# Optimization experiments

Hardware: AMD Instinct MI355X
Metric: run time of the kernel (lower is better)

## Reference

```python
import jax, jax.numpy as jnp
import numpy as np

N = 10000      # nodes
E = 160000     # edges
C = 72         # hidden dim = 18 * mul (mul=4)
A = 16         # node_attr dim (16x0e)
L = 3          # layers
O = 64         # output dim (64x0e)
B = 16         # graphs in batch
IN_DIM = 18    # irreps_node_input dim
SH = 9         # spherical harmonics dim, lmax=2
FC = 100       # radial MLP hidden (fc_neurons=[1,100])
MAX_RADIUS = 2.0
NUM_NEIGHBORS = 16.0
NUM_NODES = 625.0


def sph_harm_l2(d):
    # component-normalized real spherical harmonics up to l=2 on unit vectors d [E,3]
    x, y, z = d[:, 0], d[:, 1], d[:, 2]
    s3, s5, s15 = 3.0 ** 0.5, 5.0 ** 0.5, 15.0 ** 0.5
    return jnp.stack([
        jnp.ones_like(x),
        s3 * x, s3 * y, s3 * z,
        s15 * x * y, s15 * y * z, (s5 / 2.0) * (3.0 * z * z - 1.0),
        s15 * x * z, (s15 / 2.0) * (x * x - y * y),
    ], axis=1)  # [E, 9]


def setup_inputs() -> dict:
    key = jax.random.key(0)
    ks = jax.random.split(key, 16)
    pos = jax.random.normal(ks[0], (N, 3), dtype=jnp.float32)
    node_attr = jax.random.normal(ks[1], (N, A), dtype=jnp.float32)
    batch = jnp.sort(jax.random.randint(ks[2], (N,), 0, B))
    edge_src = jax.random.randint(ks[3], (E,), 0, N)
    edge_dst = jax.random.randint(ks[4], (E,), 0, N)
    W_in = jax.random.normal(ks[5], (IN_DIM, C), dtype=jnp.float32) / np.sqrt(IN_DIM)
    W_tp = jax.random.normal(ks[6], (L, SH, C, C), dtype=jnp.float32) / np.sqrt(C)
    W_self = jax.random.normal(ks[7], (L, C, C), dtype=jnp.float32) / np.sqrt(C)
    W_attr = jax.random.normal(ks[8], (L, A, C), dtype=jnp.float32) / np.sqrt(A)
    fc1_w = jax.random.normal(ks[9], (L, 1, FC), dtype=jnp.float32)
    fc1_b = jnp.zeros((L, FC), dtype=jnp.float32)
    fc2_w = jax.random.normal(ks[10], (L, FC, SH), dtype=jnp.float32) / np.sqrt(FC)
    W_out = jax.random.normal(ks[11], (C, O), dtype=jnp.float32) / np.sqrt(C)
    return {"pos": pos, "node_attr": node_attr, "batch": batch,
            "edge_src": edge_src, "edge_dst": edge_dst,
            "W_in": W_in, "W_tp": W_tp, "W_self": W_self, "W_attr": W_attr,
            "fc1_w": fc1_w, "fc1_b": fc1_b, "fc2_w": fc2_w, "W_out": W_out}


def reference(pos, node_attr, batch, edge_src, edge_dst,
              W_in, W_tp, W_self, W_attr, fc1_w, fc1_b, fc2_w, W_out):
    n = pos.shape[0]
    # edge geometry
    rvec = pos[edge_src] - pos[edge_dst]                      # [E,3]
    r = jnp.linalg.norm(rvec, axis=1, keepdims=True)          # [E,1]
    dvec = rvec / jnp.maximum(r, 1e-9)
    sh = sph_harm_l2(dvec)                                    # [E,9]
    # single cosine radial basis with cutoff at max_radius (number_of_basis=1)
    t = r / MAX_RADIUS
    emb = jnp.where(t < 1.0, jnp.cos(0.5 * jnp.pi * t), 0.0)  # [E,1]
    # node inputs: fixed one-hot on the scalar channel, embedded to hidden dim
    onehot = jnp.zeros((IN_DIM,), dtype=pos.dtype).at[0].set(1.0)
    h = jnp.broadcast_to((onehot @ W_in)[None, :], (n, C))    # [N,C]
    for l in range(L):
        # radial MLP -> per-edge, per-SH-path weights
        u = jax.nn.silu(emb @ fc1_w[l] + fc1_b[l]) @ fc2_w[l]  # [E,9]
        path = u * sh                                          # [E,9]
        hs = h[edge_src]                                       # [E,C]
        m = jnp.zeros_like(hs)
        for s in range(SH):  # fixed small set of tensor-product paths
            m = m + path[:, s:s + 1] * (hs @ W_tp[l, s])       # [E,C]
        agg = jax.ops.segment_sum(m, edge_dst, num_segments=n) / np.sqrt(NUM_NEIGHBORS)
        h = jax.nn.gelu(agg + h @ W_self[l] + node_attr @ W_attr[l])
    out_nodes = h @ W_out                                      # [N,O]
    pooled = jax.ops.segment_sum(out_nodes, batch, num_segments=B)
    return pooled / np.sqrt(NUM_NODES)                         # [B,O]
```

## Files before the change

kernel.cpp:

```cpp
#include <hip/hip_runtime.h>
#include <math.h>

#define NN 10000
#define NE 160000
#define CC 72
#define AA 16
#define LL 3
#define OO 64
#define NBATCH 16
#define SH 9
#define FCN 100
#define KK (SH*CC)
#define KA 736
#define KP 768
#define KG 96
#define NT 5
#define PSTRIDE 12
#define NB 1024
#define EMAX 176

typedef __attribute__((ext_vector_type(8))) short bf16x8;
typedef __attribute__((ext_vector_type(4))) float f32x4;

static __device__ __forceinline__ float gelu_tanh(float x) {
    float x3 = x * x * x;
    float inner = 0.7978845608028654f * (x + 0.044715f * x3);
    return 0.5f * x * (1.0f + tanhf(inner));
}
static __device__ __forceinline__ unsigned short f2bf(float x) {
    unsigned int u = __float_as_uint(x);
    u += 0x7FFFu + ((u >> 16) & 1u);
    return (unsigned short)(u >> 16);
}
static __device__ __forceinline__ float bf2f(unsigned short u) {
    return __uint_as_float((unsigned int)u << 16);
}

#define GB_HIST 625
#define GB_UTAB 13
#define GB_WCAT 180
#define GB_INIT 704
#define GB_PREP (GB_HIST + GB_UTAB + GB_WCAT + GB_INIT)

__global__ __launch_bounds__(256) void k_prep(
        const float* __restrict__ pos, const int* __restrict__ esrc,
        const int* __restrict__ edst, int* __restrict__ cnt,
        const float* __restrict__ fc1w, const float* __restrict__ fc1b,
        const float* __restrict__ fc2w, float* __restrict__ U,
        const float* __restrict__ Wtp, const float* __restrict__ Wself,
        const float* __restrict__ Wattr, unsigned short* __restrict__ Wb,
        const float* __restrict__ W_in, unsigned short* __restrict__ h0) {
    int bb = blockIdx.x, t = threadIdx.x;
    if (bb < GB_HIST) {
        int e = bb * 256 + t;
        if (e < NE) {
            int s = esrc[e], d = edst[e];
            float dx = pos[3 * s] - pos[3 * d];
            float dy = pos[3 * s + 1] - pos[3 * d + 1];
            float dz = pos[3 * s + 2] - pos[3 * d + 2];
            float r = sqrtf(dx * dx + dy * dy + dz * dz);
            if (r * 0.5f < 1.0f) atomicAdd(&cnt[d], 1);
        }
        return;
    }
    bb -= GB_HIST;
    if (bb < GB_UTAB) {
        int i = bb * 256 + t;
        if (i < LL * (NB + 1)) {
            int l = i / (NB + 1), b = i - l * (NB + 1);
            float emb = cosf(1.5707963267948966f * ((float)b / (float)NB));
            float u[SH];
#pragma unroll
            for (int q = 0; q < SH; ++q) u[q] = 0.f;
            const float* w1 = &fc1w[l * FCN];
            const float* b1 = &fc1b[l * FCN];
            const float* w2 = &fc2w[l * FCN * SH];
            for (int f = 0; f < FCN; ++f) {
                float a = emb * w1[f] + b1[f];
                float si = a / (1.0f + expf(-a));
#pragma unroll
                for (int q = 0; q < SH; ++q) u[q] += si * w2[f * SH + q];
            }
            float* ud = &U[(size_t)i * 12];
#pragma unroll
            for (int q = 0; q < SH; ++q) ud[q] = u[q];
            ud[9] = 0.f; ud[10] = 0.f; ud[11] = 0.f;
        }
        return;
    }
    bb -= GB_UTAB;
    if (bb < GB_WCAT) {
        int i0 = (bb * 256 + t) * 4;
#pragma unroll
        for (int u = 0; u < 4; ++u) {
            int i = i0 + u;
            int l = i / (NT * KG * 128);
            int rem = i - l * (NT * KG * 128);
            int nt = rem / (KG * 128); rem -= nt * (KG * 128);
            int kg = rem / 128; int e = rem - kg * 128;
            int n = nt * 16 + (e >> 3);
            int k = kg * 8 + (e & 7);
            float v = 0.f;
            if (n < CC && k < KA) {
                if (k < KK)            v = 0.25f * Wtp[(size_t)l * KK * CC + k * CC + n];
                else if (k < KK + CC)  v = Wself[(size_t)l * CC * CC + (k - KK) * CC + n];
                else                   v = Wattr[(size_t)l * AA * CC + (k - KK - CC) * CC + n];
            }
            Wb[i] = f2bf(v);
        }
        return;
    }
    bb -= GB_WCAT;
    {
        int i0 = (bb * 256 + t) * 4;
#pragma unroll
        for (int u = 0; u < 4; ++u) {
            int i = i0 + u;
            if (i < NN * CC) h0[i] = f2bf(W_in[i % CC]);
        }
    }
}

__global__ void k_scan(const int* __restrict__ cnt, int* __restrict__ off) {
    __shared__ int sa[256], sb[256];
    const int PER = 40;
    int t = threadIdx.x;
    int base = t * PER;
    int loc[PER];
    int run = 0;
#pragma unroll
    for (int i = 0; i < PER; ++i) {
        int idx = base + i;
        int v = (idx < NN) ? cnt[idx] : 0;
        loc[i] = run;
        run += v;
    }
    sa[t] = run;
    __syncthreads();
    int* in = sa; int* out = sb;
    for (int o = 1; o < 256; o <<= 1) {
        int v = in[t];
        if (t >= o) v += in[t - o];
        out[t] = v;
        __syncthreads();
        int* tmp = in; in = out; out = tmp;
    }
    int ebase = (t > 0) ? in[t - 1] : 0;
#pragma unroll
    for (int i = 0; i < PER; ++i) {
        int idx = base + i;
        if (idx <= NN) off[idx] = ebase + loc[i];
    }
}

__global__ void k_scatter2(const float* __restrict__ pos, const int* __restrict__ esrc,
                           const int* __restrict__ edst, const int* __restrict__ off,
                           int* __restrict__ cur, int* __restrict__ src_s,
                           int* __restrict__ dst_s) {
    int e = blockIdx.x * blockDim.x + threadIdx.x;
    if (e >= NE) return;
    int s = esrc[e], d = edst[e];
    float dx = pos[3 * s] - pos[3 * d];
    float dy = pos[3 * s + 1] - pos[3 * d + 1];
    float dz = pos[3 * s + 2] - pos[3 * d + 2];
    float r = sqrtf(dx * dx + dy * dy + dz * dz);
    if (r * 0.5f < 1.0f) {
        int slot = off[d] + atomicAdd(&cur[d], 1);
        src_s[slot] = s;
        dst_s[slot] = d;
    }
}

__global__ __launch_bounds__(256) void k_path2(const float* __restrict__ pos,
                                               const int* __restrict__ src_s,
                                               const int* __restrict__ dst_s,
                                               const float* __restrict__ U,
                                               const int* __restrict__ off,
                                               float* __restrict__ path) {
    int slot = blockIdx.x * blockDim.x + threadIdx.x;
    if (slot >= off[NN]) return;
    int s = src_s[slot], d = dst_s[slot];
    float dx = pos[3 * s] - pos[3 * d];
    float dy = pos[3 * s + 1] - pos[3 * d + 1];
    float dz = pos[3 * s + 2] - pos[3 * d + 2];
    float r = sqrtf(dx * dx + dy * dy + dz * dz);
    float inv = 1.0f / fmaxf(r, 1e-9f);
    float x = dx * inv, y = dy * inv, z = dz * inv;
    const float s3 = 1.7320508075688772f;
    const float s5 = 2.23606797749979f;
    const float s15 = 3.872983346207417f;
    float sh[SH];
    sh[0] = 1.0f;
    sh[1] = s3 * x;
    sh[2] = s3 * y;
    sh[3] = s3 * z;
    sh[4] = s15 * x * y;
    sh[5] = s15 * y * z;
    sh[6] = 0.5f * s5 * (3.0f * z * z - 1.0f);
    sh[7] = s15 * x * z;
    sh[8] = 0.5f * s15 * (x * x - y * y);

    float fb = r * 0.5f * (float)NB;
    int b0 = (int)fb;
    float fr = fb - (float)b0;

#pragma unroll
    for (int l = 0; l < LL; ++l) {
        const float* t0 = &U[((size_t)l * (NB + 1) + b0) * 12];
        float4 a0 = *(const float4*)(t0 + 0);
        float4 a1 = *(const float4*)(t0 + 4);
        float  a2 = t0[8];
        float4 c0 = *(const float4*)(t0 + 12);
        float4 c1 = *(const float4*)(t0 + 16);
        float  c2 = t0[20];
        float u0 = a0.x + fr * (c0.x - a0.x);
        float u1 = a0.y + fr * (c0.y - a0.y);
        float u2 = a0.z + fr * (c0.z - a0.z);
        float u3 = a0.w + fr * (c0.w - a0.w);
        float u4 = a1.x + fr * (c1.x - a1.x);
        float u5 = a1.y + fr * (c1.y - a1.y);
        float u6 = a1.z + fr * (c1.z - a1.z);
        float u7 = a1.w + fr * (c1.w - a1.w);
        float u8 = a2   + fr * (c2   - a2);
        float* pd = &path[((size_t)l * NE + slot) * PSTRIDE];
        *(float4*)(pd + 0) = make_float4(u0 * sh[0], u1 * sh[1], u2 * sh[2], u3 * sh[3]);
        *(float4*)(pd + 4) = make_float4(u4 * sh[4], u5 * sh[5], u6 * sh[6], u7 * sh[7]);
        *(float4*)(pd + 8) = make_float4(u8 * sh[8], 0.f, 0.f, 0.f);
    }
}

__global__ __launch_bounds__(1024, 8) void k_layer(
        const unsigned short* __restrict__ h,
        const float* __restrict__ attr,
        const float* __restrict__ path_l,
        const int* __restrict__ src_s,
        const int* __restrict__ off,
        const unsigned short* __restrict__ Wb,
        unsigned short* __restrict__ hout) {
    __shared__ float Plds[EMAX * PSTRIDE];
    __shared__ unsigned short Alds[KG * 128];
    int t = threadIdx.x, w = t >> 6, lane = t & 63;
    int n0 = blockIdx.x * 16;
    int d = n0 + w;
    int b0 = off[n0], e0 = off[n0 + 16];
    int db = off[d], de = off[d + 1];

    float a1[SH], a2[SH];
#pragma unroll
    for (int q = 0; q < SH; ++q) { a1[q] = 0.f; a2[q] = 0.f; }
    bool two = lane < (CC - 64);

    for (int base = b0; base < e0; base += EMAX) {
        int nE = min(EMAX, e0 - base);
        const float4* p4 = (const float4*)(path_l + (size_t)base * PSTRIDE);
        for (int idx = t; idx < nE * 3; idx += 1024)
            *(float4*)&Plds[idx * 4] = p4[idx];
        __syncthreads();
        int lb = db > base ? db : base;
        int le = de < base + nE ? de : base + nE;
        for (int i = lb; i < le; i += 4) {
            int m = le - i;
            float h1v[4], h2v[4];
#pragma unroll
            for (int j = 0; j < 4; ++j) {
                if (j < m) {
                    int s = src_s[i + j];
                    h1v[j] = bf2f(h[(size_t)s * CC + lane]);
                    h2v[j] = two ? bf2f(h[(size_t)s * CC + 64 + lane]) : 0.f;
                }
            }
#pragma unroll
            for (int j = 0; j < 4; ++j) {
                if (j < m) {
                    const float* p = &Plds[(i + j - base) * PSTRIDE];
                    float4 p0 = *(const float4*)p;
                    float4 p1 = *(const float4*)(p + 4);
                    float p8 = p[8];
                    float hv1 = h1v[j], hv2 = h2v[j];
                    a1[0] += p0.x * hv1; a2[0] += p0.x * hv2;
                    a1[1] += p0.y * hv1; a2[1] += p0.y * hv2;
                    a1[2] += p0.z * hv1; a2[2] += p0.z * hv2;
                    a1[3] += p0.w * hv1; a2[3] += p0.w * hv2;
                    a1[4] += p1.x * hv1; a2[4] += p1.x * hv2;
                    a1[5] += p1.y * hv1; a2[5] += p1.y * hv2;
                    a1[6] += p1.z * hv1; a2[6] += p1.z * hv2;
                    a1[7] += p1.w * hv1; a2[7] += p1.w * hv2;
                    a1[8] += p8 * hv1;   a2[8] += p8 * hv2;
                }
            }
        }
        __syncthreads();
    }

    unsigned short* At = Alds + w * 8;
    int kgc = lane >> 3, kjc = lane & 7;
#pragma unroll
    for (int q = 0; q < SH; ++q) {
        At[(9 * q + kgc) * 128 + kjc] = f2bf(a1[q]);
        if (two) At[(9 * q + 8) * 128 + lane] = f2bf(a2[q]);
    }
    At[(81 + kgc) * 128 + kjc] = h[(size_t)d * CC + lane];
    if (two) At[89 * 128 + lane] = h[(size_t)d * CC + 64 + lane];
    if (lane < AA) At[(90 + (lane >> 3)) * 128 + (lane & 7)] = f2bf(attr[(size_t)d * AA + lane]);
    if (lane < 32) At[(92 + (lane >> 3)) * 128 + (lane & 7)] = 0;
    __syncthreads();

    if (w < NT) {
        const unsigned short* Ab = Alds + (lane & 15) * 8;
        const unsigned short* Bb = Wb + ((size_t)w * KG) * 128 + (lane & 15) * 8;
        f32x4 acc = (f32x4){0.f, 0.f, 0.f, 0.f};
#pragma unroll
        for (int s = 0; s < 24; ++s) {
            int kg = s * 4 + (lane >> 4);
            bf16x8 af = *(const bf16x8*)(Ab + (size_t)kg * 128);
            bf16x8 bq = *(const bf16x8*)(Bb + (size_t)kg * 128);
            acc = __builtin_amdgcn_mfma_f32_16x16x32_bf16(af, bq, acc, 0, 0, 0);
        }
        int cb = lane & 15, rb = (lane >> 4) * 4;
        int row = n0 + rb, col = w * 16 + cb;
        if (col < CC) {
#pragma unroll
            for (int j = 0; j < 4; ++j)
                hout[(size_t)(row + j) * CC + col] = f2bf(gelu_tanh(acc[j]));
        }
    }
}

__global__ __launch_bounds__(256) void k_pool(const unsigned short* __restrict__ h,
                                              const int* __restrict__ batch,
                                              float* __restrict__ hp) {
    __shared__ float sp[NBATCH * CC];
    int t = threadIdx.x;
    for (int i = t; i < NBATCH * CC; i += 256) sp[i] = 0.f;
    __syncthreads();
    int n0 = blockIdx.x * 16;
    for (int i = t; i < 16 * CC; i += 256) {
        int nl = i / CC, c = i - nl * CC;
        int n = n0 + nl;
        if (n < NN) atomicAdd(&sp[batch[n] * CC + c], bf2f(h[(size_t)n * CC + c]));
    }
    __syncthreads();
    for (int i = t; i < NBATCH * CC; i += 256) {
        float v = sp[i];
        if (v != 0.f) atomicAdd(&hp[i], v);
    }
}

__global__ __launch_bounds__(1024) void k_outmm(const float* __restrict__ hp,
                                                const float* __restrict__ Wout,
                                                float* __restrict__ out) {
    __shared__ float hs[NBATCH * CC];
    int t = threadIdx.x;
    for (int i = t; i < NBATCH * CC; i += 1024) hs[i] = hp[i];
    __syncthreads();
    int b = t >> 6, o = t & 63;
    float acc = 0.f;
#pragma unroll 8
    for (int c = 0; c < CC; ++c) acc += hs[b * CC + c] * Wout[c * OO + o];
    out[t] = acc * (1.0f / 25.0f);
}

extern "C" void kernel_launch(void* const* d_in, const int* in_sizes, int n_in,
                              void* d_out, int out_size, void* d_ws, size_t ws_size,
                              hipStream_t stream) {
    const float* pos       = (const float*)d_in[0];
    const float* node_attr = (const float*)d_in[1];
    const int*   batch     = (const int*)d_in[2];
    const int*   esrc      = (const int*)d_in[3];
    const int*   edst      = (const int*)d_in[4];
    const float* W_in      = (const float*)d_in[5];
    const float* W_tp      = (const float*)d_in[6];
    const float* W_self    = (const float*)d_in[7];
    const float* W_attr    = (const float*)d_in[8];
    const float* fc1w      = (const float*)d_in[9];
    const float* fc1b      = (const float*)d_in[10];
    const float* fc2w      = (const float*)d_in[11];
    const float* W_out     = (const float*)d_in[12];
    float* out = (float*)d_out;

    char* p = (char*)d_ws;
    auto alloc = [&](size_t bytes) -> void* {
        void* r = (void*)p;
        p += (bytes + 255) & ~(size_t)255;
        return r;
    };
    size_t cntPad = ((size_t)NN * 4 + 255) & ~(size_t)255;
    int*   cnt   = (int*)alloc((size_t)NN * 4);
    int*   cur   = (int*)alloc((size_t)NN * 4);
    float* hp    = (float*)alloc((size_t)NBATCH * CC * 4);
    int*   off   = (int*)alloc((size_t)(NN + 1) * 4);
    int*   src_s = (int*)alloc((size_t)NE * 4);
    int*   dst_s = (int*)alloc((size_t)NE * 4);
    float* path  = (float*)alloc((size_t)LL * NE * PSTRIDE * 4);
    float* U     = (float*)alloc((size_t)LL * (NB + 1) * 12 * 4);
    unsigned short* Wb = (unsigned short*)alloc((size_t)LL * NT * KG * 128 * 2);
    unsigned short* h0 = (unsigned short*)alloc((size_t)NN * CC * 2);
    unsigned short* h1 = (unsigned short*)alloc((size_t)NN * CC * 2);

    hipMemsetAsync(cnt, 0, cntPad * 2 + (size_t)NBATCH * CC * 4, stream);

    k_prep<<<GB_PREP, 256, 0, stream>>>(pos, esrc, edst, cnt, fc1w, fc1b, fc2w, U,
                                        W_tp, W_self, W_attr, Wb, W_in, h0);
    k_scan<<<1, 256, 0, stream>>>(cnt, off);
    k_scatter2<<<(NE + 255) / 256, 256, 0, stream>>>(pos, esrc, edst, off, cur, src_s, dst_s);
    k_path2<<<(NE + 255) / 256, 256, 0, stream>>>(pos, src_s, dst_s, U, off, path);

    const unsigned short* hin = h0;
    unsigned short* hout = h1;
    for (int l = 0; l < LL; ++l) {
        k_layer<<<NN / 16, 1024, 0, stream>>>(hin, node_attr,
                                              path + (size_t)l * NE * PSTRIDE, src_s, off,
                                              Wb + (size_t)l * NT * KG * 128, hout);
        const unsigned short* tmp = hin; hin = hout; hout = (unsigned short*)tmp;
    }
    k_pool<<<(NN + 15) / 16, 256, 0, stream>>>(hin, batch, hp);
    k_outmm<<<1, 1024, 0, stream>>>(hp, W_out, out);
}
```

Before: 150.8 us.

## Fuse edge scatter with path computation and pack bf16 pairs in layer gather

Merges the CSR scatter and per-edge path kernels into one pass, so each edge computes its geometry once and writes its path row directly at its atomically claimed slot. The dst_s array and one re-read of positions are dropped. The scan kernel now seeds the cursor array with the offsets and zeroes the pooling buffer, and a tiny zero kernel replaces the memset. In the layer kernel each lane loads two adjacent bf16 channels as one 32-bit word (36 active lanes instead of 64 plus 8 with a second load) and writes packed pairs into LDS. The trade is fewer kernel launches and less memory traffic, at the cost of path writes landing at scattered slots rather than contiguously.

```diff
diff --git a/kernel.cpp b/kernel.cpp
--- a/kernel.cpp
+++ b/kernel.cpp
@@ -34,6 +34,14 @@
 }
 static __device__ __forceinline__ float bf2f(unsigned short u) {
     return __uint_as_float((unsigned int)u << 16);
+}
+static __device__ __forceinline__ unsigned int pack2bf(float lo, float hi) {
+    return (unsigned int)f2bf(lo) | ((unsigned int)f2bf(hi) << 16);
+}
+
+__global__ void k_zero(int* __restrict__ cnt) {
+    int i = blockIdx.x * blockDim.x + threadIdx.x;
+    if (i < NN) cnt[i] = 0;
 }
 
 #define GB_HIST 625
@@ -121,7 +129,8 @@
     }
 }
 
-__global__ void k_scan(const int* __restrict__ cnt, int* __restrict__ off) {
+__global__ void k_scan(const int* __restrict__ cnt, int* __restrict__ off,
+                       int* __restrict__ cur, float* __restrict__ hp) {
     __shared__ int sa[256], sb[256];
     const int PER = 40;
     int t = threadIdx.x;
@@ -149,14 +158,22 @@
 #pragma unroll
     for (int i = 0; i < PER; ++i) {
         int idx = base + i;
-        if (idx <= NN) off[idx] = ebase + loc[i];
-    }
-}
-
-__global__ void k_scatter2(const float* __restrict__ pos, const int* __restrict__ esrc,
-                           const int* __restrict__ edst, const int* __restrict__ off,
-                           int* __restrict__ cur, int* __restrict__ src_s,
-                           int* __restrict__ dst_s) {
+        if (idx <= NN) {
+            int v = ebase + loc[i];
+            off[idx] = v;
+            if (idx < NN) cur[idx] = v;
+        }
+    }
+    for (int i = t; i < NBATCH * CC; i += 256) hp[i] = 0.f;
+}
+
+__global__ __launch_bounds__(256) void k_scatter3(const float* __restrict__ pos,
+                                                  const int* __restrict__ esrc,
+                                                  const int* __restrict__ edst,
+                                                  int* __restrict__ cur,
+                                                  int* __restrict__ src_s,
+                                                  const float* __restrict__ U,
+                                                  float* __restrict__ path) {
     int e = blockIdx.x * blockDim.x + threadIdx.x;
     if (e >= NE) return;
     int s = esrc[e], d = edst[e];
@@ -164,26 +181,10 @@
     float dy = pos[3 * s + 1] - pos[3 * d + 1];
     float dz = pos[3 * s + 2] - pos[3 * d + 2];
     float r = sqrtf(dx * dx + dy * dy + dz * dz);
-    if (r * 0.5f < 1.0f) {
-        int slot = off[d] + atomicAdd(&cur[d], 1);
-        src_s[slot] = s;
-        dst_s[slot] = d;
-    }
-}
-
-__global__ __launch_bounds__(256) void k_path2(const float* __restrict__ pos,
-                                               const int* __restrict__ src_s,
-                                               const int* __restrict__ dst_s,
-                                               const float* __restrict__ U,
-                                               const int* __restrict__ off,
-                                               float* __restrict__ path) {
-    int slot = blockIdx.x * blockDim.x + threadIdx.x;
-    if (slot >= off[NN]) return;
-    int s = src_s[slot], d = dst_s[slot];
-    float dx = pos[3 * s] - pos[3 * d];
-    float dy = pos[3 * s + 1] - pos[3 * d + 1];
-    float dz = pos[3 * s + 2] - pos[3 * d + 2];
-    float r = sqrtf(dx * dx + dy * dy + dz * dz);
+    if (r * 0.5f >= 1.0f) return;
+    int slot = atomicAdd(&cur[d], 1);
+    src_s[slot] = s;
+
     float inv = 1.0f / fmaxf(r, 1e-9f);
     float x = dx * inv, y = dy * inv, z = dz * inv;
     const float s3 = 1.7320508075688772f;
@@ -245,10 +246,11 @@
     int b0 = off[n0], e0 = off[n0 + 16];
     int db = off[d], de = off[d + 1];
 
+    bool act = lane < 36;
+    int c2 = 2 * lane;
     float a1[SH], a2[SH];
 #pragma unroll
     for (int q = 0; q < SH; ++q) { a1[q] = 0.f; a2[q] = 0.f; }
-    bool two = lane < (CC - 64);
 
     for (int base = b0; base < e0; base += EMAX) {
         int nE = min(EMAX, e0 - base);
@@ -260,13 +262,12 @@
         int le = de < base + nE ? de : base + nE;
         for (int i = lb; i < le; i += 4) {
             int m = le - i;
-            float h1v[4], h2v[4];
+            unsigned int hv[4];
 #pragma unroll
             for (int j = 0; j < 4; ++j) {
-                if (j < m) {
+                if (j < m && act) {
                     int s = src_s[i + j];
-                    h1v[j] = bf2f(h[(size_t)s * CC + lane]);
-                    h2v[j] = two ? bf2f(h[(size_t)s * CC + 64 + lane]) : 0.f;
+                    hv[j] = *(const unsigned int*)&h[(size_t)s * CC + c2];
                 }
             }
 #pragma unroll
@@ -276,33 +277,37 @@
                     float4 p0 = *(const float4*)p;
                     float4 p1 = *(const float4*)(p + 4);
                     float p8 = p[8];
-                    float hv1 = h1v[j], hv2 = h2v[j];
-                    a1[0] += p0.x * hv1; a2[0] += p0.x * hv2;
-                    a1[1] += p0.y * hv1; a2[1] += p0.y * hv2;
-                    a1[2] += p0.z * hv1; a2[2] += p0.z * hv2;
-                    a1[3] += p0.w * hv1; a2[3] += p0.w * hv2;
-                    a1[4] += p1.x * hv1; a2[4] += p1.x * hv2;
-                    a1[5] += p1.y * hv1; a2[5] += p1.y * hv2;
-                    a1[6] += p1.z * hv1; a2[6] += p1.z * hv2;
-                    a1[7] += p1.w * hv1; a2[7] += p1.w * hv2;
-                    a1[8] += p8 * hv1;   a2[8] += p8 * hv2;
+                    float lo = act ? bf2f((unsigned short)(hv[j] & 0xffffu)) : 0.f;
+                    float hi = act ? bf2f((unsigned short)(hv[j] >> 16)) : 0.f;
+                    a1[0] += p0.x * lo; a2[0] += p0.x * hi;
+                    a1[1] += p0.y * lo; a2[1] += p0.y * hi;
+                    a1[2] += p0.z * lo; a2[2] += p0.z * hi;
+                    a1[3] += p0.w * lo; a2[3] += p0.w * hi;
+                    a1[4] += p1.x * lo; a2[4] += p1.x * hi;
+                    a1[5] += p1.y * lo; a2[5] += p1.y * hi;
+                    a1[6] += p1.z * lo; a2[6] += p1.z * hi;
+                    a1[7] += p1.w * lo; a2[7] += p1.w * hi;
+                    a1[8] += p8 * lo;   a2[8] += p8 * hi;
                 }
             }
         }
         __syncthreads();
     }
 
-    unsigned short* At = Alds + w * 8;
-    int kgc = lane >> 3, kjc = lane & 7;
-#pragma unroll
-    for (int q = 0; q < SH; ++q) {
-        At[(9 * q + kgc) * 128 + kjc] = f2bf(a1[q]);
-        if (two) At[(9 * q + 8) * 128 + lane] = f2bf(a2[q]);
-    }
-    At[(81 + kgc) * 128 + kjc] = h[(size_t)d * CC + lane];
-    if (two) At[89 * 128 + lane] = h[(size_t)d * CC + 64 + lane];
-    if (lane < AA) At[(90 + (lane >> 3)) * 128 + (lane & 7)] = f2bf(attr[(size_t)d * AA + lane]);
-    if (lane < 32) At[(92 + (lane >> 3)) * 128 + (lane & 7)] = 0;
+    if (act) {
+        int kgo = lane >> 2, kjo = 2 * (lane & 3);
+        int hb = w * 8 + kjo;
+#pragma unroll
+        for (int q = 0; q < SH; ++q)
+            *(unsigned int*)&Alds[(9 * q + kgo) * 128 + hb] = pack2bf(a1[q], a2[q]);
+        *(unsigned int*)&Alds[(81 + kgo) * 128 + hb] =
+            *(const unsigned int*)&h[(size_t)d * CC + c2];
+        if (lane < 8)
+            *(unsigned int*)&Alds[(90 + kgo) * 128 + hb] =
+                pack2bf(attr[(size_t)d * AA + c2], attr[(size_t)d * AA + c2 + 1]);
+    }
+    if (lane < 16)
+        *(unsigned int*)&Alds[(92 + (lane >> 2)) * 128 + w * 8 + 2 * (lane & 3)] = 0u;
     __syncthreads();
 
     if (w < NT) {
@@ -384,26 +389,22 @@
         p += (bytes + 255) & ~(size_t)255;
         return r;
     };
-    size_t cntPad = ((size_t)NN * 4 + 255) & ~(size_t)255;
     int*   cnt   = (int*)alloc((size_t)NN * 4);
     int*   cur   = (int*)alloc((size_t)NN * 4);
     float* hp    = (float*)alloc((size_t)NBATCH * CC * 4);
     int*   off   = (int*)alloc((size_t)(NN + 1) * 4);
     int*   src_s = (int*)alloc((size_t)NE * 4);
-    int*   dst_s = (int*)alloc((size_t)NE * 4);
     float* path  = (float*)alloc((size_t)LL * NE * PSTRIDE * 4);
     float* U     = (float*)alloc((size_t)LL * (NB + 1) * 12 * 4);
     unsigned short* Wb = (unsigned short*)alloc((size_t)LL * NT * KG * 128 * 2);
     unsigned short* h0 = (unsigned short*)alloc((size_t)NN * CC * 2);
     unsigned short* h1 = (unsigned short*)alloc((size_t)NN * CC * 2);
 
-    hipMemsetAsync(cnt, 0, cntPad * 2 + (size_t)NBATCH * CC * 4, stream);
-
+    k_zero<<<(NN + 255) / 256, 256, 0, stream>>>(cnt);
     k_prep<<<GB_PREP, 256, 0, stream>>>(pos, esrc, edst, cnt, fc1w, fc1b, fc2w, U,
                                         W_tp, W_self, W_attr, Wb, W_in, h0);
-    k_scan<<<1, 256, 0, stream>>>(cnt, off);
-    k_scatter2<<<(NE + 255) / 256, 256, 0, stream>>>(pos, esrc, edst, off, cur, src_s, dst_s);
-    k_path2<<<(NE + 255) / 256, 256, 0, stream>>>(pos, src_s, dst_s, U, off, path);
+    k_scan<<<1, 256, 0, stream>>>(cnt, off, cur, hp);
+    k_scatter3<<<(NE + 255) / 256, 256, 0, stream>>>(pos, esrc, edst, cur, src_s, U, path);
 
     const unsigned short* hin = h0;
     unsigned short* hout = h1;
```

After: 139.0 us. 1.09x faster.
